# Kernel optimization log

Measured on AMD Instinct MI355X. Metric: run time of the kernel, lower is better.

The kernel has to match this reference:

```python
import jax, jax.numpy as jnp
import numpy as np

HEADS = 16
DIM = 1024
HEAD_DIM = DIM // HEADS


def setup_inputs() -> dict:
    key = jax.random.key(0)
    k1, k2 = jax.random.split(key)
    images = jax.random.normal(k1, (2, 2048, DIM), dtype=jnp.float32)
    # torch nn.Linear(dim, 3*dim, bias=False): y = x @ W.T, W: [3*dim, dim].
    # Store as [dim, 3*dim] for direct x @ W_qkv.
    W_qkv = jax.random.normal(k2, (DIM, 3 * DIM), dtype=jnp.float32) / np.sqrt(DIM)
    return {"images": images, "W_qkv": W_qkv}


def reference(images, W_qkv):
    B, S, D = images.shape
    qkv = images @ W_qkv  # [B, S, 3D]
    q, k, v = jnp.split(qkv, 3, axis=-1)
    # [B, S, H, Dh] -> [B, H, S, Dh]
    def to_heads(t):
        return t.reshape(B, S, HEADS, HEAD_DIM).transpose(0, 2, 1, 3)
    q, k, v = to_heads(q), to_heads(k), to_heads(v)
    scale = 1.0 / jnp.sqrt(jnp.asarray(HEAD_DIM, dtype=q.dtype))
    scores = jnp.einsum('bhqd,bhkd->bhqk', q, k) * scale  # [B, H, S, S]
    probs = jax.nn.softmax(scores, axis=-1)
    out = jnp.einsum('bhqk,bhkd->bhqd', probs, v)  # [B, H, S, Dh]
    return out.transpose(0, 2, 1, 3).reshape(B, S, D)
```

## Files before the change

kernel.cpp:

```cpp
#include <hip/hip_runtime.h>
#include <hip/hip_bf16.h>
#include <math.h>

typedef __bf16 bf16x8 __attribute__((ext_vector_type(8)));
typedef float f32x4 __attribute__((ext_vector_type(4)));
typedef unsigned short u16x8 __attribute__((ext_vector_type(8)));
typedef unsigned short u16;

#define S_LEN 2048
#define DMODEL 1024
#define NH 16

__device__ __forceinline__ u16 f2bf(float f) {
    __bf16 b = (__bf16)f;
    return __builtin_bit_cast(u16, b);
}
__device__ __forceinline__ float bf2f(u16 u) {
    union { unsigned int i; float f; } v; v.i = ((unsigned int)u) << 16; return v.f;
}

__device__ __forceinline__ void gload16(const u16* g, u16* lds_base) {
    __builtin_amdgcn_global_load_lds(
        (const __attribute__((address_space(1))) unsigned int*)g,
        (__attribute__((address_space(3))) unsigned int*)lds_base,
        16, 0, 0);
}

__global__ __launch_bounds__(256) void cvt_x(const float* __restrict__ in, u16* __restrict__ outp) {
    int i = (blockIdx.x * 256 + threadIdx.x) * 4;
    float4 v = *(const float4*)(in + i);
    outp[i + 0] = f2bf(v.x); outp[i + 1] = f2bf(v.y);
    outp[i + 2] = f2bf(v.z); outp[i + 3] = f2bf(v.w);
}

__global__ __launch_bounds__(256) void transpose_w(const float* __restrict__ W, u16* __restrict__ Wt) {
    __shared__ u16 tile[32][33];
    int n0 = blockIdx.x * 32, k0 = blockIdx.y * 32;
    int tx = threadIdx.x & 31, ty = threadIdx.x >> 5;
#pragma unroll
    for (int i = 0; i < 4; i++) {
        int k = ty + i * 8;
        tile[k][tx] = f2bf(W[(size_t)(k0 + k) * 3072 + n0 + tx]);
    }
    __syncthreads();
#pragma unroll
    for (int i = 0; i < 4; i++) {
        int n = ty + i * 8;
        Wt[(size_t)(n0 + n) * 1024 + k0 + tx] = tile[tx][n];
    }
}

__global__ __launch_bounds__(256) void qkv_gemm(const u16* __restrict__ A, const u16* __restrict__ Bt,
                                                u16* __restrict__ C) {
    __shared__ alignas(16) u16 As[128 * 64];
    __shared__ alignas(16) u16 Bs[128 * 64];
    const int tid = threadIdx.x, l = tid & 63, w = tid >> 6;
    const int bm = blockIdx.y, bn = blockIdx.x;
    const int wm = w >> 1, wn = w & 1;
    const int c0 = l & 15, g = l >> 4;
    f32x4 acc[4][4] = {};
    for (int kt = 0; kt < 1024; kt += 64) {
        __syncthreads();
#pragma unroll
        for (int n = 0; n < 4; n++) {
            int i = tid + n * 256;
            int r = i >> 3, c = i & 7;
            int cs = c ^ (r & 7);
            u16* dstA = As + (size_t)(w * 64 + n * 256) * 8;
            u16* dstB = Bs + (size_t)(w * 64 + n * 256) * 8;
            gload16(A + (size_t)(bm * 128 + r) * 1024 + kt + cs * 8, dstA);
            gload16(Bt + (size_t)(bn * 128 + r) * 1024 + kt + cs * 8, dstB);
        }
        __syncthreads();
#pragma unroll
        for (int kk = 0; kk < 2; kk++) {
            bf16x8 af[4], bfr[4];
#pragma unroll
            for (int m = 0; m < 4; m++) {
                int row = wm * 64 + m * 16 + c0;
                af[m] = *(const bf16x8*)((const char*)As + row * 128 + (((g + kk * 4) ^ (row & 7)) << 4));
            }
#pragma unroll
            for (int n = 0; n < 4; n++) {
                int row = wn * 64 + n * 16 + c0;
                bfr[n] = *(const bf16x8*)((const char*)Bs + row * 128 + (((g + kk * 4) ^ (row & 7)) << 4));
            }
#pragma unroll
            for (int m = 0; m < 4; m++)
#pragma unroll
                for (int n = 0; n < 4; n++)
                    acc[m][n] = __builtin_amdgcn_mfma_f32_16x16x32_bf16(af[m], bfr[n], acc[m][n], 0, 0, 0);
        }
    }
#pragma unroll
    for (int m = 0; m < 4; m++)
#pragma unroll
        for (int n = 0; n < 4; n++)
#pragma unroll
            for (int j = 0; j < 4; j++) {
                int row = bm * 128 + wm * 64 + m * 16 + 4 * g + j;
                int col = bn * 128 + wn * 64 + n * 16 + c0;
                C[(size_t)row * 3072 + col] = f2bf(acc[m][n][j]);
            }
}

__global__ __launch_bounds__(256) void transpose_v(const u16* __restrict__ QKV, u16* __restrict__ Vtp) {
    __shared__ u16 tile[64][72];
    const int bh = blockIdx.x >> 5, st = blockIdx.x & 31;
    const int b = bh >> 4, h = bh & 15;
    const u16* src = QKV + (size_t)b * S_LEN * 3072 + 2048 + h * 64;
    const int sl = threadIdx.x >> 2;
    const int cg = (threadIdx.x & 3) * 16;
#pragma unroll
    for (int ii = 0; ii < 2; ii++) {
        u16x8 v = *(const u16x8*)(src + (size_t)(st * 64 + sl) * 3072 + cg + ii * 8);
        *(u16x8*)&tile[sl][cg + ii * 8] = v;
    }
    __syncthreads();
    const int dl = threadIdx.x >> 2;
#pragma unroll
    for (int ii = 0; ii < 2; ii++) {
        u16x8 o;
#pragma unroll
        for (int q = 0; q < 8; q++) {
            int p = cg + ii * 8 + q;
            int kb = 2 * (p >> 5) + ((p >> 2) & 1);
            int t = kb * 16 + ((p >> 3) & 3) * 4 + (p & 3);
            o[q] = tile[t][dl];
        }
        *(u16x8*)(Vtp + ((size_t)bh * 64 + dl) * S_LEN + st * 64 + cg + ii * 8) = o;
    }
}

__global__ __launch_bounds__(128, 2) void attn5(const u16* __restrict__ QKV, const u16* __restrict__ Vtp,
                                                float* __restrict__ out) {
    __shared__ alignas(16) u16 Ks[2][64 * 64];
    __shared__ alignas(16) u16 Vs[2][64 * 64];
    const int bid = blockIdx.x;
    const int wg = ((bid & 7) << 7) | (bid >> 3);
    const int tid = threadIdx.x, l = tid & 63, w = tid >> 6;
    const int qt = wg & 31, bh = wg >> 5;
    const int b = bh >> 4, h = bh & 15;
    const int c0 = l & 15, g = l >> 4;
    const u16* Qb = QKV + (size_t)b * S_LEN * 3072 + h * 64;
    const u16* Kb = Qb + 1024;
    const u16* Vb = Vtp + (size_t)bh * 64 * S_LEN;

    int rr[4], cc[4];
#pragma unroll
    for (int n = 0; n < 4; n++) {
        int i = tid + n * 128;
        rr[n] = i >> 3;
        cc[n] = ((i & 7) ^ (rr[n] & 7)) * 8;
    }

    int koff[8], voff[8];
#pragma unroll
    for (int kb = 0; kb < 4; kb++)
#pragma unroll
        for (int kk = 0; kk < 2; kk++) {
            int key = kb * 16 + c0;
            koff[kb * 2 + kk] = key * 128 + (((g + kk * 4) ^ (key & 7)) << 4);
        }
#pragma unroll
    for (int kk = 0; kk < 2; kk++)
#pragma unroll
        for (int n = 0; n < 4; n++) {
            int d = n * 16 + c0;
            voff[kk * 4 + n] = d * 128 + (((g + 4 * kk) ^ (d & 7)) << 4);
        }

    bf16x8 qf[2][2];
    {
        const float qs = 0.125f * 1.44269504f;
#pragma unroll
        for (int s = 0; s < 2; s++) {
            int qrow = qt * 64 + w * 32 + s * 16 + c0;
#pragma unroll
            for (int kk = 0; kk < 2; kk++) {
                u16x8 v = *(const u16x8*)(Qb + (size_t)qrow * 3072 + kk * 32 + g * 8);
                bf16x8 q;
#pragma unroll
                for (int j = 0; j < 8; j++) q[j] = (__bf16)(bf2f(v[j]) * qs);
                qf[s][kk] = q;
            }
        }
    }
    bf16x8 vone;
#pragma unroll
    for (int j = 0; j < 8; j++) vone[j] = (__bf16)1.0f;

    float m_r[2] = {-INFINITY, -INFINITY};
    f32x4 accO[2][4] = {};
    f32x4 accL[2] = {};

#pragma unroll
    for (int n = 0; n < 4; n++) {
        gload16(Kb + (size_t)rr[n] * 3072 + cc[n], Ks[0] + (size_t)(w * 64 + n * 128) * 8);
        gload16(Vb + (size_t)rr[n] * S_LEN + cc[n], Vs[0] + (size_t)(w * 64 + n * 128) * 8);
    }

    for (int t = 0; t < 32; t++) {
        const int cur = t & 1;
        __syncthreads();
        if (t + 1 < 32) {
            const int kvn = (t + 1) * 64;
#pragma unroll
            for (int n = 0; n < 4; n++) {
                gload16(Kb + (size_t)(kvn + rr[n]) * 3072 + cc[n], Ks[cur ^ 1] + (size_t)(w * 64 + n * 128) * 8);
                gload16(Vb + (size_t)rr[n] * S_LEN + kvn + cc[n], Vs[cur ^ 1] + (size_t)(w * 64 + n * 128) * 8);
            }
        }
        const char* Kc = (const char*)Ks[cur];
        const char* Vc = (const char*)Vs[cur];
        f32x4 sc[2][4] = {};
        __builtin_amdgcn_s_setprio(1);
#pragma unroll
        for (int kb = 0; kb < 4; kb++)
#pragma unroll
            for (int kk = 0; kk < 2; kk++) {
                bf16x8 kf = *(const bf16x8*)(Kc + koff[kb * 2 + kk]);
                sc[0][kb] = __builtin_amdgcn_mfma_f32_16x16x32_bf16(kf, qf[0][kk], sc[0][kb], 0, 0, 0);
                sc[1][kb] = __builtin_amdgcn_mfma_f32_16x16x32_bf16(kf, qf[1][kk], sc[1][kb], 0, 0, 0);
            }
        __builtin_amdgcn_s_setprio(0);
        bf16x8 vf[2][4];
#pragma unroll
        for (int kk = 0; kk < 2; kk++)
#pragma unroll
            for (int n = 0; n < 4; n++)
                vf[kk][n] = *(const bf16x8*)(Vc + voff[kk * 4 + n]);
#pragma unroll
        for (int s = 0; s < 2; s++) {
            float m0 = fmaxf(fmaxf(sc[s][0][0], sc[s][0][1]), sc[s][0][2]);
            float m1 = fmaxf(fmaxf(sc[s][0][3], sc[s][1][0]), sc[s][1][1]);
            float m2 = fmaxf(fmaxf(sc[s][1][2], sc[s][1][3]), sc[s][2][0]);
            float m3 = fmaxf(fmaxf(sc[s][2][1], sc[s][2][2]), sc[s][2][3]);
            float m4 = fmaxf(fmaxf(sc[s][3][0], sc[s][3][1]), sc[s][3][2]);
            float mx = fmaxf(fmaxf(fmaxf(m0, m1), m2), fmaxf(fmaxf(m3, m4), sc[s][3][3]));
            mx = fmaxf(mx, __shfl_xor(mx, 16));
            mx = fmaxf(mx, __shfl_xor(mx, 32));
            if (!__all(mx <= m_r[s] + 8.f)) {
                float mnew = fmaxf(m_r[s], mx);
                float alpha = __builtin_amdgcn_exp2f(m_r[s] - mnew);
                m_r[s] = mnew;
#pragma unroll
                for (int j = 0; j < 4; j++) {
                    float aj = __shfl(alpha, 20 * g + j);
                    accL[s][j] *= aj;
#pragma unroll
                    for (int n = 0; n < 4; n++) accO[s][n][j] *= aj;
                }
            }
#pragma unroll
            for (int kb = 0; kb < 4; kb++)
#pragma unroll
                for (int j = 0; j < 4; j++)
                    sc[s][kb][j] = __builtin_amdgcn_exp2f(sc[s][kb][j] - m_r[s]);
            __builtin_amdgcn_s_setprio(1);
#pragma unroll
            for (int kk = 0; kk < 2; kk++) {
                bf16x8 pf;
#pragma unroll
                for (int j = 0; j < 4; j++) {
                    pf[j]     = (__bf16)sc[s][2 * kk][j];
                    pf[j + 4] = (__bf16)sc[s][2 * kk + 1][j];
                }
                accL[s] = __builtin_amdgcn_mfma_f32_16x16x32_bf16(pf, vone, accL[s], 0, 0, 0);
#pragma unroll
                for (int n = 0; n < 4; n++)
                    accO[s][n] = __builtin_amdgcn_mfma_f32_16x16x32_bf16(pf, vf[kk][n], accO[s][n], 0, 0, 0);
            }
            __builtin_amdgcn_s_setprio(0);
        }
    }
#pragma unroll
    for (int s = 0; s < 2; s++)
#pragma unroll
        for (int j = 0; j < 4; j++) {
            float inv = 1.0f / accL[s][j];
            int row = qt * 64 + w * 32 + s * 16 + 4 * g + j;
#pragma unroll
            for (int n = 0; n < 4; n++)
                out[((size_t)b * S_LEN + row) * DMODEL + h * 64 + n * 16 + c0] = accO[s][n][j] * inv;
        }
}

extern "C" void kernel_launch(void* const* d_in, const int* in_sizes, int n_in,
                              void* d_out, int out_size, void* d_ws, size_t ws_size,
                              hipStream_t stream) {
    const float* X = (const float*)d_in[0];
    const float* W = (const float*)d_in[1];
    float* out = (float*)d_out;

    u16* Xb  = (u16*)d_ws;
    u16* Wt  = Xb + (size_t)4096 * 1024;
    u16* QKV = Wt + (size_t)3072 * 1024;
    u16* Vtp = QKV + (size_t)4096 * 3072;

    cvt_x<<<4096, 256, 0, stream>>>(X, Xb);
    transpose_w<<<dim3(96, 32), 256, 0, stream>>>(W, Wt);
    qkv_gemm<<<dim3(24, 32), 256, 0, stream>>>(Xb, Wt, QKV);
    transpose_v<<<1024, 256, 0, stream>>>(QKV, Vtp);
    attn5<<<1024, 128, 0, stream>>>(QKV, Vtp, out);
}
```

Baseline: 112.7 us.

## Split attention KV range in two halves and merge partial results

Attention blocks now use 256 threads covering 128 query rows each, and every block handles only half of the key/value sequence (split-K, flash-decoding style). The first half writes its normalized output straight to the final buffer, and the second half writes an fp16 partial plus per-row max and sum. A new merge kernel then combines the two halves. The aim is shorter per-block loops and more waves per CU, paid for with an extra kernel launch, extra global traffic for partials, and fp16 rounding of the second half's output.

```diff
diff --git a/kernel.cpp b/kernel.cpp
--- a/kernel.cpp
+++ b/kernel.cpp
@@ -5,11 +5,13 @@
 typedef __bf16 bf16x8 __attribute__((ext_vector_type(8)));
 typedef float f32x4 __attribute__((ext_vector_type(4)));
 typedef unsigned short u16x8 __attribute__((ext_vector_type(8)));
+typedef _Float16 h16x4 __attribute__((ext_vector_type(4)));
 typedef unsigned short u16;
 
 #define S_LEN 2048
 #define DMODEL 1024
 #define NH 16
+#define NROWS 65536
 
 __device__ __forceinline__ u16 f2bf(float f) {
     __bf16 b = (__bf16)f;
@@ -132,27 +134,27 @@
     }
 }
 
-__global__ __launch_bounds__(128, 2) void attn5(const u16* __restrict__ QKV, const u16* __restrict__ Vtp,
-                                                float* __restrict__ out) {
+__global__ __launch_bounds__(256, 4) void attn6(const u16* __restrict__ QKV, const u16* __restrict__ Vtp,
+                                                float* __restrict__ outp, _Float16* __restrict__ Op1,
+                                                float* __restrict__ Mp, float* __restrict__ Lp) {
     __shared__ alignas(16) u16 Ks[2][64 * 64];
     __shared__ alignas(16) u16 Vs[2][64 * 64];
     const int bid = blockIdx.x;
     const int wg = ((bid & 7) << 7) | (bid >> 3);
     const int tid = threadIdx.x, l = tid & 63, w = tid >> 6;
-    const int qt = wg & 31, bh = wg >> 5;
+    const int bh = wg >> 5, rest = wg & 31;
+    const int qt = rest >> 1, hf = rest & 1;
     const int b = bh >> 4, h = bh & 15;
     const int c0 = l & 15, g = l >> 4;
     const u16* Qb = QKV + (size_t)b * S_LEN * 3072 + h * 64;
     const u16* Kb = Qb + 1024;
     const u16* Vb = Vtp + (size_t)bh * 64 * S_LEN;
-
-    int rr[4], cc[4];
-#pragma unroll
-    for (int n = 0; n < 4; n++) {
-        int i = tid + n * 128;
-        rr[n] = i >> 3;
-        cc[n] = ((i & 7) ^ (rr[n] & 7)) * 8;
-    }
+    const int kv0 = hf * 1024;
+
+    const int rA = tid >> 3, cA = ((tid & 7) ^ (rA & 7)) * 8;
+    const int i1 = tid + 256;
+    const int rB = i1 >> 3, cB = ((i1 & 7) ^ (rB & 7)) * 8;
+    const int dbA = (w * 64) * 8, dbB = (256 + w * 64) * 8;
 
     int koff[8], voff[8];
 #pragma unroll
@@ -175,7 +177,7 @@
         const float qs = 0.125f * 1.44269504f;
 #pragma unroll
         for (int s = 0; s < 2; s++) {
-            int qrow = qt * 64 + w * 32 + s * 16 + c0;
+            int qrow = qt * 128 + w * 32 + s * 16 + c0;
 #pragma unroll
             for (int kk = 0; kk < 2; kk++) {
                 u16x8 v = *(const u16x8*)(Qb + (size_t)qrow * 3072 + kk * 32 + g * 8);
@@ -194,22 +196,20 @@
     f32x4 accO[2][4] = {};
     f32x4 accL[2] = {};
 
-#pragma unroll
-    for (int n = 0; n < 4; n++) {
-        gload16(Kb + (size_t)rr[n] * 3072 + cc[n], Ks[0] + (size_t)(w * 64 + n * 128) * 8);
-        gload16(Vb + (size_t)rr[n] * S_LEN + cc[n], Vs[0] + (size_t)(w * 64 + n * 128) * 8);
-    }
-
-    for (int t = 0; t < 32; t++) {
+    gload16(Kb + (size_t)(kv0 + rA) * 3072 + cA, Ks[0] + dbA);
+    gload16(Kb + (size_t)(kv0 + rB) * 3072 + cB, Ks[0] + dbB);
+    gload16(Vb + (size_t)rA * S_LEN + kv0 + cA, Vs[0] + dbA);
+    gload16(Vb + (size_t)rB * S_LEN + kv0 + cB, Vs[0] + dbB);
+
+    for (int t = 0; t < 16; t++) {
         const int cur = t & 1;
         __syncthreads();
-        if (t + 1 < 32) {
-            const int kvn = (t + 1) * 64;
-#pragma unroll
-            for (int n = 0; n < 4; n++) {
-                gload16(Kb + (size_t)(kvn + rr[n]) * 3072 + cc[n], Ks[cur ^ 1] + (size_t)(w * 64 + n * 128) * 8);
-                gload16(Vb + (size_t)rr[n] * S_LEN + kvn + cc[n], Vs[cur ^ 1] + (size_t)(w * 64 + n * 128) * 8);
-            }
+        if (t + 1 < 16) {
+            const int kvn = kv0 + (t + 1) * 64;
+            gload16(Kb + (size_t)(kvn + rA) * 3072 + cA, Ks[cur ^ 1] + dbA);
+            gload16(Kb + (size_t)(kvn + rB) * 3072 + cB, Ks[cur ^ 1] + dbB);
+            gload16(Vb + (size_t)rA * S_LEN + kvn + cA, Vs[cur ^ 1] + dbA);
+            gload16(Vb + (size_t)rB * S_LEN + kvn + cB, Vs[cur ^ 1] + dbB);
         }
         const char* Kc = (const char*)Ks[cur];
         const char* Vc = (const char*)Vs[cur];
@@ -275,15 +275,61 @@
         }
     }
 #pragma unroll
-    for (int s = 0; s < 2; s++)
-#pragma unroll
-        for (int j = 0; j < 4; j++) {
-            float inv = 1.0f / accL[s][j];
-            int row = qt * 64 + w * 32 + s * 16 + 4 * g + j;
-#pragma unroll
-            for (int n = 0; n < 4; n++)
-                out[((size_t)b * S_LEN + row) * DMODEL + h * 64 + n * 16 + c0] = accO[s][n][j] * inv;
-        }
+    for (int s = 0; s < 2; s++) {
+        const int rowbase = qt * 128 + w * 32 + s * 16;
+        const int rowg0 = bh * 2048 + rowbase;
+        if (hf == 0) {
+#pragma unroll
+            for (int j = 0; j < 4; j++) {
+                float inv = 1.0f / accL[s][j];
+                int row = rowbase + 4 * g + j;
+                float* op = outp + ((size_t)b * S_LEN + row) * DMODEL + h * 64;
+#pragma unroll
+                for (int n = 0; n < 4; n++) op[n * 16 + c0] = accO[s][n][j] * inv;
+            }
+        } else {
+#pragma unroll
+            for (int j = 0; j < 4; j++) {
+                float inv = 1.0f / accL[s][j];
+                size_t rg = (size_t)(rowg0 + 4 * g + j) * 64;
+#pragma unroll
+                for (int n = 0; n < 4; n++) Op1[rg + n * 16 + c0] = (_Float16)(accO[s][n][j] * inv);
+            }
+        }
+        if (g == 0) Mp[hf * NROWS + rowg0 + c0] = m_r[s];
+        if (c0 == 0) {
+#pragma unroll
+            for (int j = 0; j < 4; j++) Lp[hf * NROWS + rowg0 + 4 * g + j] = accL[s][j];
+        }
+    }
+}
+
+__global__ __launch_bounds__(256) void attn_merge(float* __restrict__ outp, const _Float16* __restrict__ Op1,
+                                                  const float* __restrict__ Mp, const float* __restrict__ Lp) {
+    int t = blockIdx.x * 256 + threadIdx.x;
+    int r = t >> 2;
+    int dc = (t & 3) * 16;
+    int bh = r >> 11, srow = r & 2047;
+    int b = bh >> 4, h = bh & 15;
+    float m0 = Mp[r], m1 = Mp[NROWS + r];
+    float l0 = Lp[r], l1 = Lp[NROWS + r];
+    float M = fmaxf(m0, m1);
+    float w0 = __builtin_amdgcn_exp2f(m0 - M) * l0;
+    float w1 = __builtin_amdgcn_exp2f(m1 - M) * l1;
+    float inv = 1.0f / (w0 + w1);
+    float a0 = w0 * inv, a1 = w1 * inv;
+    float* op = outp + ((size_t)b * S_LEN + srow) * DMODEL + h * 64 + dc;
+    const _Float16* o1 = Op1 + (size_t)r * 64 + dc;
+#pragma unroll
+    for (int q = 0; q < 4; q++) {
+        float4 v0 = *(const float4*)(op + q * 4);
+        h16x4 v1 = *(const h16x4*)(o1 + q * 4);
+        v0.x = a0 * v0.x + a1 * (float)v1[0];
+        v0.y = a0 * v0.y + a1 * (float)v1[1];
+        v0.z = a0 * v0.z + a1 * (float)v1[2];
+        v0.w = a0 * v0.w + a1 * (float)v1[3];
+        *(float4*)(op + q * 4) = v0;
+    }
 }
 
 extern "C" void kernel_launch(void* const* d_in, const int* in_sizes, int n_in,
@@ -297,10 +343,14 @@
     u16* Wt  = Xb + (size_t)4096 * 1024;
     u16* QKV = Wt + (size_t)3072 * 1024;
     u16* Vtp = QKV + (size_t)4096 * 3072;
+    _Float16* Op1 = (_Float16*)Xb;
+    float* Mp = (float*)Wt;
+    float* Lp = Mp + 2 * NROWS;
 
     cvt_x<<<4096, 256, 0, stream>>>(X, Xb);
     transpose_w<<<dim3(96, 32), 256, 0, stream>>>(W, Wt);
     qkv_gemm<<<dim3(24, 32), 256, 0, stream>>>(Xb, Wt, QKV);
     transpose_v<<<1024, 256, 0, stream>>>(QKV, Vtp);
-    attn5<<<1024, 128, 0, stream>>>(QKV, Vtp, out);
-}
+    attn6<<<1024, 256, 0, stream>>>(QKV, Vtp, out, Op1, Mp, Lp);
+    attn_merge<<<1024, 256, 0, stream>>>(out, Op1, Mp, Lp);
+}
```

Measured after the change: 126.6 us. +12.3%, slower.
